# Kernel optimization log

Hardware: AMD Instinct MI355X
Metric: run time of the kernel (lower is better)

The kernel has to match this reference:

```python
import jax, jax.numpy as jnp
import numpy as np

VERY_NEG = -1e30

H = 768           # hidden_size
A_DIM = 768       # attention_dim_size
N_TREE = 40000    # num_tree_nodes (embed_init vocab)
N_CODES = 10000   # number of leaf codes (rows of leaves_list)
MAX_ANC = 8       # max ancestors per code
B, V, M = 16, 32, 48  # batch, visits, codes per visit
OUT = 512         # classifier output_size


def setup_inputs() -> dict:
    key = jax.random.key(0)
    ks = jax.random.split(key, 12)
    leaves_list = jax.random.randint(ks[0], (N_CODES, MAX_ANC), 0, N_TREE)
    ancestors_list = jax.random.randint(ks[1], (N_CODES, MAX_ANC), 0, N_TREE)
    masks = (jax.random.uniform(ks[2], (N_CODES, MAX_ANC)) > 0.3).astype(jnp.float32)
    masks = masks.at[:, 0].set(1.0)  # ensure at least one valid ancestor
    input_ids = jax.random.randint(ks[3], (B, V, M), 0, N_CODES + 1)  # 0 is padding row
    code_mask = (jax.random.uniform(ks[4], (B, V, M)) > 0.2).astype(jnp.float32)
    code_mask = code_mask.at[:, :, 0].set(1.0)
    s = 1.0 / np.sqrt(H)
    embed_table = jax.random.normal(ks[5], (N_TREE, H), dtype=jnp.float32) * s
    w1 = jax.random.normal(ks[6], (2 * H, A_DIM), dtype=jnp.float32) * (1.0 / np.sqrt(2 * H))
    b1 = jnp.zeros((A_DIM,), dtype=jnp.float32)
    w2 = jax.random.normal(ks[7], (A_DIM, 1), dtype=jnp.float32) * (1.0 / np.sqrt(A_DIM))
    b2 = jnp.zeros((1,), dtype=jnp.float32)
    wc = jax.random.normal(ks[8], (H, OUT), dtype=jnp.float32) * s
    bc = jnp.zeros((OUT,), dtype=jnp.float32)
    return {
        "embed_table": embed_table, "w1": w1, "b1": b1, "w2": w2, "b2": b2,
        "wc": wc, "bc": bc, "masks": masks, "code_mask": code_mask,
        "leaves_list": leaves_list, "ancestors_list": ancestors_list,
        "input_ids": input_ids,
    }


def reference(embed_table, w1, b1, w2, b2, wc, bc, masks, code_mask,
              leaves_list, ancestors_list, input_ids):
    # --- DAGAttention2D over ancestor axis ---
    leaves = embed_table[leaves_list]        # [N, A, H]
    ancestors = embed_table[ancestors_list]  # [N, A, H]
    m = masks[:, :, None]                    # [N, A, 1]
    x = jnp.concatenate([leaves * m, ancestors * m], axis=-1)  # [N, A, 2H]
    x = jax.nn.relu(jnp.einsum('nah,hd->nad', x, w1) + b1)
    x = jnp.einsum('nad,do->nao', x, w2) + b2                  # [N, A, 1]
    x = x + (1.0 - m) * VERY_NEG
    attn = jax.nn.softmax(x, axis=1)                           # softmax over ancestors
    dag_emb = (attn * ancestors * m).sum(axis=1)               # [N, H]
    # --- dict_matrix with padding row 0, embedding lookup ---
    dict_matrix = jnp.concatenate([jnp.zeros((1, dag_emb.shape[1]), dag_emb.dtype), dag_emb], axis=0)
    emb = dict_matrix[input_ids]             # [B, V, M, H]
    cm = code_mask[..., None]
    pooled = (emb * cm).sum(axis=2) / jnp.clip(cm.sum(axis=2), 1.0, None)  # [B, V, H]
    # --- Classifier (dropout inactive at eval, activation=None) ---
    out = jnp.einsum('bvh,ho->bvo', pooled, wc) + bc           # [B, V, OUT]
    return out
```

## Files before the change

### kernel.cpp

```cpp
#include <hip/hip_runtime.h>
#include <stdint.h>

typedef unsigned short u16;
typedef __bf16 bfx8 __attribute__((ext_vector_type(8)));
typedef float f32x4 __attribute__((ext_vector_type(4)));

#define HD 768
#define NTREE 40000
#define NCODES 10000
#define GNN 1536
#define OUTD 512
#define NBV 512
#define VNEG (-1e30f)
#define TB 4

#define BM 256
#define BN 256
#define BK 64
#define NKT (HD / BK)
#define NMT ((NTREE + BM - 1) / BM)
#define NNT (GNN / BN)
#define GRID (NMT * NNT)
#define Q8 (GRID / 8)
#define R8 (GRID % 8)

#define WAITV(n) asm volatile("s_waitcnt vmcnt(" #n ")" ::: "memory")
#define LGKM(n)  asm volatile("s_waitcnt lgkmcnt(" #n ")" ::: "memory")

__device__ __forceinline__ float bf2f(u16 u) {
  union { uint32_t i; float f; } v; v.i = ((uint32_t)u) << 16; return v.f;
}
__device__ __forceinline__ u16 f2bf(float f) {
  union { float fl; uint32_t i; } v; v.fl = f;
  uint32_t u = v.i;
  u += 0x7FFFu + ((u >> 16) & 1u);
  return (u16)(u >> 16);
}

#define NBLK_CONV 30000
__global__ void k_prep(const float* __restrict__ E, u16* __restrict__ Ebf,
                       const float* __restrict__ w1, u16* __restrict__ Bt) {
  const int bid = blockIdx.x, tid = threadIdx.x;
  if (bid < NBLK_CONV) {
    const int i = bid * 256 + tid;
    float4 v = ((const float4*)E)[i];
    ushort4 r;
    r.x = f2bf(v.x); r.y = f2bf(v.y); r.z = f2bf(v.z); r.w = f2bf(v.w);
    ((ushort4*)Ebf)[i] = r;
  } else {
    const int idx = (bid - NBLK_CONV) * 256 + tid;
    if (idx < GNN * HD) {
      const int n = idx / HD, k = idx % HD;
      const int srow = k + ((n >= HD) ? HD : 0);
      const int scol = (n >= HD) ? (n - HD) : n;
      Bt[idx] = f2bf(w1[(size_t)srow * HD + scol]);
    }
  }
}

__global__ __launch_bounds__(512, 2) void k_gemm(const u16* __restrict__ A,
                                                 const u16* __restrict__ B,
                                                 u16* __restrict__ C) {
  __shared__ u16 lds[65536];

  const int tid    = threadIdx.x;
  const int lane   = tid & 63;
  const int wv     = tid >> 6;
  const int wr     = wv >> 2;
  const int wc     = wv & 3;
  const int lane15 = lane & 15;
  const int g      = lane >> 4;

  const int orig = blockIdx.x;
  const int xcd = orig & 7, lin = orig >> 3;
  const int wg = (xcd < R8 ? xcd * (Q8 + 1) : R8 * (Q8 + 1) + (xcd - R8) * Q8) + lin;
  const int mt = wg / NNT, nt = wg % NNT;
  const int tm = mt * BM, tn = nt * BN;

  uint32_t aOff[2][2], bOff[2][2];
#pragma unroll
  for (int u = 0; u < 2; ++u) {
    const int o    = u * 8192 + tid * 16;
    const int rloc = o >> 7;
    const int c    = ((o >> 4) & 7) ^ (rloc & 7);
#pragma unroll
    for (int h = 0; h < 2; ++h) {
      int ra = tm + h * 128 + rloc; if (ra > NTREE - 1) ra = NTREE - 1;
      aOff[u][h] = (uint32_t)ra * HD + c * 8;
      bOff[u][h] = (uint32_t)(tn + h * 128 + rloc) * HD + c * 8;
    }
  }

#define STAGE_A(MH, NB, TT) do {                                               \
    _Pragma("unroll") for (int u = 0; u < 2; ++u)                              \
      __builtin_amdgcn_global_load_lds(                                        \
        (const __attribute__((address_space(1))) void*)(A + aOff[u][MH] + (TT) * BK), \
        (__attribute__((address_space(3))) void*)((char*)lds + (NB) * 32768 +  \
            (MH) * 16384 + u * 8192 + tid * 16),                               \
        16, 0, 0);                                                             \
  } while (0)

#define STAGE_B(NH, NB, TT) do {                                               \
    _Pragma("unroll") for (int u = 0; u < 2; ++u)                              \
      __builtin_amdgcn_global_load_lds(                                        \
        (const __attribute__((address_space(1))) void*)(B + bOff[u][NH] + (TT) * BK), \
        (__attribute__((address_space(3))) void*)((char*)lds + 65536 +         \
            (NB) * 32768 + (NH) * 16384 + u * 8192 + tid * 16),                \
        16, 0, 0);                                                             \
  } while (0)

  f32x4 acc[4][4][2];
#pragma unroll
  for (int q = 0; q < 4; ++q)
#pragma unroll
    for (int i = 0; i < 4; ++i)
#pragma unroll
      for (int j = 0; j < 2; ++j) acc[q][i][j] = (f32x4){0.f, 0.f, 0.f, 0.f};

  int colz[2];
  colz[0] = ((0 * 4 + g) ^ (lane15 & 7)) * 8;
  colz[1] = ((1 * 4 + g) ^ (lane15 & 7)) * 8;
  const int aLane = wr * 4096 + lane15 * 64;
  const int bLane = wc * 2048 + lane15 * 64;

  bfx8 aF[4][2], bF[2][2];

#define READ_A(MH, BA) do {                                                    \
    _Pragma("unroll") for (int mf = 0; mf < 4; ++mf)                           \
      _Pragma("unroll") for (int ks = 0; ks < 2; ++ks)                         \
        aF[mf][ks] = *(const bfx8*)&lds[(BA) + (MH) * 8192 + aLane +           \
                                        mf * 1024 + colz[ks]];                 \
  } while (0)

#define READ_B(NH, BB) do {                                                    \
    _Pragma("unroll") for (int nf = 0; nf < 2; ++nf)                           \
      _Pragma("unroll") for (int ks = 0; ks < 2; ++ks)                         \
        bF[nf][ks] = *(const bfx8*)&lds[(BB) + (NH) * 8192 + bLane +           \
                                        nf * 1024 + colz[ks]];                 \
  } while (0)

#define MFMA_Q(Q) do {                                                         \
    LGKM(0);                                                                   \
    __builtin_amdgcn_sched_barrier(0);                                         \
    __builtin_amdgcn_s_setprio(1);                                             \
    _Pragma("unroll") for (int mf = 0; mf < 4; ++mf)                           \
      _Pragma("unroll") for (int nf = 0; nf < 2; ++nf)                         \
        _Pragma("unroll") for (int ks = 0; ks < 2; ++ks)                       \
          acc[Q][mf][nf] = __builtin_amdgcn_mfma_f32_16x16x32_bf16(            \
              aF[mf][ks], bF[nf][ks], acc[Q][mf][nf], 0, 0, 0);                \
    __builtin_amdgcn_s_setprio(0);                                             \
  } while (0)

  STAGE_A(0, 0, 0);
  STAGE_B(0, 0, 0);
  STAGE_B(1, 0, 0);
  STAGE_A(1, 0, 0);
  WAITV(4);
  __builtin_amdgcn_s_barrier();

  for (int t = 0; t < NKT; ++t) {
    const int bA = (t & 1) * 16384;
    const int bB = 32768 + (t & 1) * 16384;
    const int nb = (t + 1) & 1;
    const bool more = (t + 1 < NKT);

    READ_A(0, bA);
    READ_B(0, bB);
    if (more) STAGE_A(0, nb, t + 1);
    MFMA_Q(0);
    if (more) { WAITV(4); } else { WAITV(2); }
    __builtin_amdgcn_s_barrier();

    READ_B(1, bB);
    if (more) STAGE_B(0, nb, t + 1);
    MFMA_Q(1);
    if (more) { WAITV(4); } else { WAITV(0); }
    __builtin_amdgcn_s_barrier();

    READ_A(1, bA);
    if (more) STAGE_B(1, nb, t + 1);
    MFMA_Q(2);
    __builtin_amdgcn_s_barrier();

    READ_B(0, bB);
    if (more) STAGE_A(1, nb, t + 1);
    MFMA_Q(3);
    if (more) { WAITV(4); }
    __builtin_amdgcn_s_barrier();
  }

  const int r0 = (lane >> 4) * 4, cc = lane15;
  const int qmh[4] = {0, 0, 1, 1}, qnh[4] = {0, 1, 1, 0};
#pragma unroll
  for (int q = 0; q < 4; ++q) {
#pragma unroll
    for (int mf = 0; mf < 4; ++mf) {
#pragma unroll
      for (int nf = 0; nf < 2; ++nf) {
#pragma unroll
        for (int rr = 0; rr < 4; ++rr) {
          const int row = tm + qmh[q] * 128 + wr * 64 + mf * 16 + r0 + rr;
          if (row < NTREE) {
            const int col = tn + qnh[q] * 128 + wc * 32 + nf * 16 + cc;
            C[(size_t)row * GNN + col] = f2bf(acc[q][mf][nf][rr]);
          }
        }
      }
    }
  }
#undef MFMA_Q
#undef READ_A
#undef READ_B
#undef STAGE_A
#undef STAGE_B
}

__global__ __launch_bounds__(512) void k_attn(const u16* __restrict__ PQ,
                                              const u16* __restrict__ Ebf,
                                              const float* __restrict__ b1,
                                              const float* __restrict__ w2,
                                              const float* __restrict__ b2,
                                              const float* __restrict__ masks,
                                              const int* __restrict__ leaves,
                                              const int* __restrict__ anc,
                                              u16* __restrict__ dag) {
  const int n = blockIdx.x;
  const int tid = threadIdx.x, lane = tid & 63, wv = tid >> 6;
  __shared__ float sc[8];
  __shared__ float m_s[8];
  __shared__ int   an_s[8];
  __shared__ int   lv_s[8];
  if (tid < 8) {
    an_s[tid] = anc[n * 8 + tid];
    lv_s[tid] = leaves[n * 8 + tid];
    m_s[tid]  = masks[n * 8 + tid];
  }
  __syncthreads();

  {
    const int a = wv;
    const float mm = m_s[a];
    if (mm == 0.f) {
      if (lane == 0) sc[a] = VNEG;
    } else {
      const int l = lv_s[a], an = an_s[a];
      const u16* pr = PQ + (size_t)l * GNN;
      const u16* qr = PQ + (size_t)an * GNN + HD;
      const int d0 = lane * 12;
      float s = 0.f;
#pragma unroll
      for (int jj = 0; jj < 3; ++jj) {
        const int d = d0 + jj * 4;
        ushort4 pv = *(const ushort4*)(pr + d);
        ushort4 qv = *(const ushort4*)(qr + d);
        float4  bb = *(const float4*)(b1 + d);
        float4  ww = *(const float4*)(w2 + d);
        float v;
        v = fmaxf(bf2f(pv.x) + bf2f(qv.x) + bb.x, 0.f); s += v * ww.x;
        v = fmaxf(bf2f(pv.y) + bf2f(qv.y) + bb.y, 0.f); s += v * ww.y;
        v = fmaxf(bf2f(pv.z) + bf2f(qv.z) + bb.z, 0.f); s += v * ww.z;
        v = fmaxf(bf2f(pv.w) + bf2f(qv.w) + bb.w, 0.f); s += v * ww.w;
      }
#pragma unroll
      for (int off = 32; off > 0; off >>= 1) s += __shfl_down(s, off);
      if (lane == 0) sc[a] = s + b2[0];
    }
  }
  __syncthreads();

  float mx = sc[0];
#pragma unroll
  for (int a = 1; a < 8; ++a) mx = fmaxf(mx, sc[a]);
  float ex[8], den = 0.f;
#pragma unroll
  for (int a = 0; a < 8; ++a) { ex[a] = expf(sc[a] - mx); den += ex[a]; }
  const float inv = 1.0f / den;
  float cf[8];
#pragma unroll
  for (int a = 0; a < 8; ++a) cf[a] = ex[a] * inv * m_s[a];

  if (tid < 384) {
    const int d = tid * 2;
    float a0 = 0.f, a1 = 0.f;
#pragma unroll
    for (int a = 0; a < 8; ++a) {
      const float cfa = cf[a];
      if (cfa != 0.f) {
        const uint32_t w = *(const uint32_t*)(Ebf + (size_t)an_s[a] * HD + d);
        a0 += cfa * bf2f((u16)(w & 0xffffu));
        a1 += cfa * bf2f((u16)(w >> 16));
      }
    }
    const uint32_t packed = (uint32_t)f2bf(a0) | ((uint32_t)f2bf(a1) << 16);
    *(uint32_t*)(dag + (size_t)n * HD + d) = packed;
  }
}

__global__ __launch_bounds__(256) void k_pool(const u16* __restrict__ dag,
                                              const int* __restrict__ ids,
                                              const float* __restrict__ cm,
                                              float* __restrict__ pooled) {
  const int bv = blockIdx.x, tid = threadIdx.x;
  __shared__ int   id_s[48];
  __shared__ float cm_s[48];
  if (tid < 48) { id_s[tid] = ids[bv * 48 + tid]; cm_s[tid] = cm[bv * 48 + tid]; }
  __syncthreads();
  float cnt = 0.f;
  for (int m = 0; m < 48; ++m) cnt += cm_s[m];
  const float scale = 1.0f / fmaxf(cnt, 1.0f);
  if (tid < 192) {
    float4 accv = make_float4(0.f, 0.f, 0.f, 0.f);
    for (int m = 0; m < 48; ++m) {
      const int id = id_s[m];
      const float cv = cm_s[m];
      if (id > 0 && cv != 0.f) {
        ushort4 v = *(const ushort4*)(dag + (size_t)(id - 1) * HD + tid * 4);
        accv.x += cv * bf2f(v.x); accv.y += cv * bf2f(v.y);
        accv.z += cv * bf2f(v.z); accv.w += cv * bf2f(v.w);
      }
    }
    accv.x *= scale; accv.y *= scale; accv.z *= scale; accv.w *= scale;
    *(float4*)(pooled + (size_t)bv * HD + tid * 4) = accv;
  }
}

__global__ __launch_bounds__(256) void k_out(const float* __restrict__ pooled,
                                             const float* __restrict__ wc,
                                             const float* __restrict__ bc,
                                             float* __restrict__ out) {
  const int b0 = blockIdx.x * TB;
  const int tid = threadIdx.x;
  __shared__ float pl[TB][HD];
  for (int i = tid; i < TB * HD; i += 256) pl[i / HD][i % HD] = pooled[(size_t)b0 * HD + i];
  __syncthreads();
  float a0[TB], a1[TB];
#pragma unroll
  for (int r = 0; r < TB; ++r) { a0[r] = 0.f; a1[r] = 0.f; }
  for (int h = 0; h < HD; ++h) {
    const float w0  = wc[(size_t)h * OUTD + tid];
    const float w1v = wc[(size_t)h * OUTD + tid + 256];
#pragma unroll
    for (int r = 0; r < TB; ++r) { const float p = pl[r][h]; a0[r] += p * w0; a1[r] += p * w1v; }
  }
  const float bc0 = bc[tid], bc1 = bc[tid + 256];
#pragma unroll
  for (int r = 0; r < TB; ++r) {
    out[(size_t)(b0 + r) * OUTD + tid]       = a0[r] + bc0;
    out[(size_t)(b0 + r) * OUTD + tid + 256] = a1[r] + bc1;
  }
}

extern "C" void kernel_launch(void* const* d_in, const int* in_sizes, int n_in,
                              void* d_out, int out_size, void* d_ws, size_t ws_size,
                              hipStream_t stream) {
  const float* E     = (const float*)d_in[0];
  const float* w1    = (const float*)d_in[1];
  const float* b1    = (const float*)d_in[2];
  const float* w2    = (const float*)d_in[3];
  const float* b2    = (const float*)d_in[4];
  const float* wc    = (const float*)d_in[5];
  const float* bc    = (const float*)d_in[6];
  const float* masks = (const float*)d_in[7];
  const float* cm    = (const float*)d_in[8];
  const int*   leaves = (const int*)d_in[9];
  const int*   anc    = (const int*)d_in[10];
  const int*   ids    = (const int*)d_in[11];
  float* out = (float*)d_out;

  if (n_in < 12) return;
  if (in_sizes[0] != NTREE * HD) return;
  if (out_size != NBV * OUTD) return;

  char* ws = (char*)d_ws;
  const size_t szEbf = (size_t)NTREE * HD * 2;
  const size_t szBt  = (size_t)GNN * HD * 2;
  const size_t szPQ  = (size_t)NTREE * GNN * 2;
  const size_t szDag = (size_t)NCODES * HD * 2;
  const size_t szPl  = (size_t)NBV * HD * 4;
  if (ws_size < szEbf + szBt + szPQ + szDag + szPl) return;

  u16*   Ebf    = (u16*)ws;            ws += szEbf;
  u16*   Bt     = (u16*)ws;            ws += szBt;
  u16*   PQ     = (u16*)ws;            ws += szPQ;
  u16*   dag    = (u16*)ws;            ws += szDag;
  float* pooled = (float*)ws;          ws += szPl;

  const int nPrep = NBLK_CONV + (GNN * HD + 255) / 256;
  k_prep<<<nPrep, 256, 0, stream>>>(E, Ebf, w1, Bt);
  k_gemm<<<GRID, 512, 0, stream>>>(Ebf, Bt, PQ);
  k_attn<<<NCODES, 512, 0, stream>>>(PQ, Ebf, b1, w2, b2, masks, leaves, anc, dag);
  k_pool<<<NBV, 256, 0, stream>>>(dag, ids, cm, pooled);
  k_out<<<NBV / TB, 256, 0, stream>>>(pooled, wc, bc, out);
}
```

Before: 277.0 us.

## Retile projection GEMM, vectorize attention score loads, and tile classifier GEMM

The main bf16 GEMM moves from 256x256x64 tiles with 512 threads and double buffering to 128x256x32 tiles with 256 threads and a three-stage LDS ring buffer, changing the swizzle and the wait/barrier schedule. The attention kernel now loads PQ rows as 8-wide and 4-wide vectors per lane instead of three 4-wide loads, so it issues fewer memory instructions. The classifier kernel becomes a shared-memory tiled 64x64 GEMM over 64 blocks in place of the row-strip loop. Together these aim to improve GEMM occupancy and latency hiding and to raise parallelism in the small final GEMM, at the cost of lower per-block reuse in the main GEMM.

```diff
diff --git a/kernel.cpp b/kernel.cpp
--- a/kernel.cpp
+++ b/kernel.cpp
@@ -4,6 +4,7 @@
 typedef unsigned short u16;
 typedef __bf16 bfx8 __attribute__((ext_vector_type(8)));
 typedef float f32x4 __attribute__((ext_vector_type(4)));
+typedef u16 u16x8 __attribute__((ext_vector_type(8)));
 
 #define HD 768
 #define NTREE 40000
@@ -12,20 +13,18 @@
 #define OUTD 512
 #define NBV 512
 #define VNEG (-1e30f)
-#define TB 4
-
-#define BM 256
-#define BN 256
-#define BK 64
-#define NKT (HD / BK)
-#define NMT ((NTREE + BM - 1) / BM)
-#define NNT (GNN / BN)
-#define GRID (NMT * NNT)
-#define Q8 (GRID / 8)
-#define R8 (GRID % 8)
+
+#define BM2 128
+#define BN2 256
+#define BK2 32
+#define NKT2 (HD / BK2)
+#define NMT2 ((NTREE + BM2 - 1) / BM2)
+#define NNT2 (GNN / BN2)
+#define GRID2 (NMT2 * NNT2)
+#define Q82 (GRID2 / 8)
+#define R82 (GRID2 % 8)
 
 #define WAITV(n) asm volatile("s_waitcnt vmcnt(" #n ")" ::: "memory")
-#define LGKM(n)  asm volatile("s_waitcnt lgkmcnt(" #n ")" ::: "memory")
 
 __device__ __forceinline__ float bf2f(u16 u) {
   union { uint32_t i; float f; } v; v.i = ((uint32_t)u) << 16; return v.f;
@@ -58,161 +57,145 @@
   }
 }
 
-__global__ __launch_bounds__(512, 2) void k_gemm(const u16* __restrict__ A,
+__global__ __launch_bounds__(256, 2) void k_gemm(const u16* __restrict__ A,
                                                  const u16* __restrict__ B,
                                                  u16* __restrict__ C) {
-  __shared__ u16 lds[65536];
+  __shared__ u16 lds[36864];
 
   const int tid    = threadIdx.x;
   const int lane   = tid & 63;
   const int wv     = tid >> 6;
-  const int wr     = wv >> 2;
-  const int wc     = wv & 3;
+  const int wr     = wv >> 1;
+  const int wc     = wv & 1;
   const int lane15 = lane & 15;
   const int g      = lane >> 4;
 
   const int orig = blockIdx.x;
   const int xcd = orig & 7, lin = orig >> 3;
-  const int wg = (xcd < R8 ? xcd * (Q8 + 1) : R8 * (Q8 + 1) + (xcd - R8) * Q8) + lin;
-  const int mt = wg / NNT, nt = wg % NNT;
-  const int tm = mt * BM, tn = nt * BN;
-
-  uint32_t aOff[2][2], bOff[2][2];
+  const int wg = (xcd < R82 ? xcd * (Q82 + 1)
+                            : R82 * (Q82 + 1) + (xcd - R82) * Q82) + lin;
+  const int mt = wg / NNT2, nt = wg % NNT2;
+  const int tm = mt * BM2, tn = nt * BN2;
+
+  uint32_t aOff[2], bOff[4];
 #pragma unroll
   for (int u = 0; u < 2; ++u) {
-    const int o    = u * 8192 + tid * 16;
-    const int rloc = o >> 7;
-    const int c    = ((o >> 4) & 7) ^ (rloc & 7);
-#pragma unroll
-    for (int h = 0; h < 2; ++h) {
-      int ra = tm + h * 128 + rloc; if (ra > NTREE - 1) ra = NTREE - 1;
-      aOff[u][h] = (uint32_t)ra * HD + c * 8;
-      bOff[u][h] = (uint32_t)(tn + h * 128 + rloc) * HD + c * 8;
-    }
-  }
-
-#define STAGE_A(MH, NB, TT) do {                                               \
+    const int idx = u * 256 + tid;
+    const int r = idx >> 2, ph = idx & 3, c = ph ^ (r & 3);
+    int ra = tm + r; if (ra > NTREE - 1) ra = NTREE - 1;
+    aOff[u] = (uint32_t)ra * HD + c * 8;
+  }
+#pragma unroll
+  for (int u = 0; u < 4; ++u) {
+    const int idx = u * 256 + tid;
+    const int r = idx >> 2, ph = idx & 3, c = ph ^ (r & 3);
+    bOff[u] = (uint32_t)(tn + r) * HD + c * 8;
+  }
+
+#define GLL(SRC, DSTBYTE)                                                      \
+  __builtin_amdgcn_global_load_lds(                                            \
+      (const __attribute__((address_space(1))) void*)(SRC),                    \
+      (__attribute__((address_space(3))) void*)((char*)lds + (DSTBYTE)),       \
+      16, 0, 0)
+
+#define STAGE_A(TT, BI) do {                                                   \
     _Pragma("unroll") for (int u = 0; u < 2; ++u)                              \
-      __builtin_amdgcn_global_load_lds(                                        \
-        (const __attribute__((address_space(1))) void*)(A + aOff[u][MH] + (TT) * BK), \
-        (__attribute__((address_space(3))) void*)((char*)lds + (NB) * 32768 +  \
-            (MH) * 16384 + u * 8192 + tid * 16),                               \
-        16, 0, 0);                                                             \
+      GLL(A + aOff[u] + (TT) * BK2, (BI) * 24576 + (u * 256 + tid) * 16);      \
   } while (0)
-
-#define STAGE_B(NH, NB, TT) do {                                               \
-    _Pragma("unroll") for (int u = 0; u < 2; ++u)                              \
-      __builtin_amdgcn_global_load_lds(                                        \
-        (const __attribute__((address_space(1))) void*)(B + bOff[u][NH] + (TT) * BK), \
-        (__attribute__((address_space(3))) void*)((char*)lds + 65536 +         \
-            (NB) * 32768 + (NH) * 16384 + u * 8192 + tid * 16),                \
-        16, 0, 0);                                                             \
+#define STAGE_BE(TT, BI) do {                                                  \
+    _Pragma("unroll") for (int u = 0; u < 4; u += 2)                           \
+      GLL(B + bOff[u] + (TT) * BK2,                                            \
+          (BI) * 24576 + 8192 + (u * 256 + tid) * 16);                         \
   } while (0)
-
-  f32x4 acc[4][4][2];
-#pragma unroll
-  for (int q = 0; q < 4; ++q)
-#pragma unroll
-    for (int i = 0; i < 4; ++i)
-#pragma unroll
-      for (int j = 0; j < 2; ++j) acc[q][i][j] = (f32x4){0.f, 0.f, 0.f, 0.f};
-
-  int colz[2];
-  colz[0] = ((0 * 4 + g) ^ (lane15 & 7)) * 8;
-  colz[1] = ((1 * 4 + g) ^ (lane15 & 7)) * 8;
-  const int aLane = wr * 4096 + lane15 * 64;
-  const int bLane = wc * 2048 + lane15 * 64;
-
-  bfx8 aF[4][2], bF[2][2];
-
-#define READ_A(MH, BA) do {                                                    \
-    _Pragma("unroll") for (int mf = 0; mf < 4; ++mf)                           \
-      _Pragma("unroll") for (int ks = 0; ks < 2; ++ks)                         \
-        aF[mf][ks] = *(const bfx8*)&lds[(BA) + (MH) * 8192 + aLane +           \
-                                        mf * 1024 + colz[ks]];                 \
+#define STAGE_BO(TT, BI) do {                                                  \
+    _Pragma("unroll") for (int u = 1; u < 4; u += 2)                           \
+      GLL(B + bOff[u] + (TT) * BK2,                                            \
+          (BI) * 24576 + 8192 + (u * 256 + tid) * 16);                         \
   } while (0)
 
-#define READ_B(NH, BB) do {                                                    \
-    _Pragma("unroll") for (int nf = 0; nf < 2; ++nf)                           \
-      _Pragma("unroll") for (int ks = 0; ks < 2; ++ks)                         \
-        bF[nf][ks] = *(const bfx8*)&lds[(BB) + (NH) * 8192 + bLane +           \
-                                        nf * 1024 + colz[ks]];                 \
-  } while (0)
-
-#define MFMA_Q(Q) do {                                                         \
-    LGKM(0);                                                                   \
-    __builtin_amdgcn_sched_barrier(0);                                         \
-    __builtin_amdgcn_s_setprio(1);                                             \
-    _Pragma("unroll") for (int mf = 0; mf < 4; ++mf)                           \
-      _Pragma("unroll") for (int nf = 0; nf < 2; ++nf)                         \
-        _Pragma("unroll") for (int ks = 0; ks < 2; ++ks)                       \
-          acc[Q][mf][nf] = __builtin_amdgcn_mfma_f32_16x16x32_bf16(            \
-              aF[mf][ks], bF[nf][ks], acc[Q][mf][nf], 0, 0, 0);                \
-    __builtin_amdgcn_s_setprio(0);                                             \
-  } while (0)
-
-  STAGE_A(0, 0, 0);
-  STAGE_B(0, 0, 0);
-  STAGE_B(1, 0, 0);
-  STAGE_A(1, 0, 0);
-  WAITV(4);
+  f32x4 acc[4][8];
+#pragma unroll
+  for (int i = 0; i < 4; ++i)
+#pragma unroll
+    for (int j = 0; j < 8; ++j) acc[i][j] = (f32x4){0.f, 0.f, 0.f, 0.f};
+
+  int aIdx[4], bIdx[8];
+#pragma unroll
+  for (int mf = 0; mf < 4; ++mf) {
+    const int R = wr * 64 + mf * 16 + lane15;
+    aIdx[mf] = R * 32 + ((g ^ (R & 3)) << 3);
+  }
+#pragma unroll
+  for (int nf = 0; nf < 8; ++nf) {
+    const int R = wc * 128 + nf * 16 + lane15;
+    bIdx[nf] = 4096 + R * 32 + ((g ^ (R & 3)) << 3);
+  }
+
+  STAGE_A(0, 0); STAGE_BE(0, 0); STAGE_BO(0, 0);
+  STAGE_A(1, 1); STAGE_BE(1, 1); STAGE_BO(1, 1);
+  WAITV(8);
   __builtin_amdgcn_s_barrier();
 
-  for (int t = 0; t < NKT; ++t) {
-    const int bA = (t & 1) * 16384;
-    const int bB = 32768 + (t & 1) * 16384;
-    const int nb = (t + 1) & 1;
-    const bool more = (t + 1 < NKT);
-
-    READ_A(0, bA);
-    READ_B(0, bB);
-    if (more) STAGE_A(0, nb, t + 1);
-    MFMA_Q(0);
-    if (more) { WAITV(4); } else { WAITV(2); }
+  int rb = 0, sb = 2;
+  for (int t = 0; t < NKT2; ++t) {
+    const int bu = rb * 12288;
+    const bool more = (t + 2 < NKT2);
+    bfx8 aF[4], bF[4], bG[4];
+
+#pragma unroll
+    for (int mf = 0; mf < 4; ++mf) aF[mf] = *(const bfx8*)&lds[bu + aIdx[mf]];
+#pragma unroll
+    for (int nf = 0; nf < 4; ++nf) bF[nf] = *(const bfx8*)&lds[bu + bIdx[nf]];
+    if (more) STAGE_A(t + 2, sb);
+    __builtin_amdgcn_s_setprio(1);
+#pragma unroll
+    for (int mf = 0; mf < 4; ++mf)
+#pragma unroll
+      for (int nf = 0; nf < 4; ++nf)
+        acc[mf][nf] = __builtin_amdgcn_mfma_f32_16x16x32_bf16(
+            aF[mf], bF[nf], acc[mf][nf], 0, 0, 0);
+    __builtin_amdgcn_s_setprio(0);
+    if (t < NKT2 - 2) { WAITV(8); } else { WAITV(0); }
     __builtin_amdgcn_s_barrier();
 
-    READ_B(1, bB);
-    if (more) STAGE_B(0, nb, t + 1);
-    MFMA_Q(1);
-    if (more) { WAITV(4); } else { WAITV(0); }
+#pragma unroll
+    for (int nf = 0; nf < 4; ++nf) bG[nf] = *(const bfx8*)&lds[bu + bIdx[4 + nf]];
+    if (more) { STAGE_BE(t + 2, sb); STAGE_BO(t + 2, sb); }
+    __builtin_amdgcn_s_setprio(1);
+#pragma unroll
+    for (int mf = 0; mf < 4; ++mf)
+#pragma unroll
+      for (int nf = 0; nf < 4; ++nf)
+        acc[mf][4 + nf] = __builtin_amdgcn_mfma_f32_16x16x32_bf16(
+            aF[mf], bG[nf], acc[mf][4 + nf], 0, 0, 0);
+    __builtin_amdgcn_s_setprio(0);
+    if (t < NKT2 - 2) { WAITV(8); }
+    else if (t == NKT2 - 2) { WAITV(0); }
     __builtin_amdgcn_s_barrier();
 
-    READ_A(1, bA);
-    if (more) STAGE_B(1, nb, t + 1);
-    MFMA_Q(2);
-    __builtin_amdgcn_s_barrier();
-
-    READ_B(0, bB);
-    if (more) STAGE_A(1, nb, t + 1);
-    MFMA_Q(3);
-    if (more) { WAITV(4); }
-    __builtin_amdgcn_s_barrier();
-  }
-
-  const int r0 = (lane >> 4) * 4, cc = lane15;
-  const int qmh[4] = {0, 0, 1, 1}, qnh[4] = {0, 1, 1, 0};
-#pragma unroll
-  for (int q = 0; q < 4; ++q) {
-#pragma unroll
-    for (int mf = 0; mf < 4; ++mf) {
-#pragma unroll
-      for (int nf = 0; nf < 2; ++nf) {
-#pragma unroll
-        for (int rr = 0; rr < 4; ++rr) {
-          const int row = tm + qmh[q] * 128 + wr * 64 + mf * 16 + r0 + rr;
-          if (row < NTREE) {
-            const int col = tn + qnh[q] * 128 + wc * 32 + nf * 16 + cc;
-            C[(size_t)row * GNN + col] = f2bf(acc[q][mf][nf][rr]);
-          }
+    rb = (rb == 2) ? 0 : rb + 1;
+    sb = (sb == 2) ? 0 : sb + 1;
+  }
+
+  const int r0 = (lane >> 4) * 4;
+#pragma unroll
+  for (int mf = 0; mf < 4; ++mf) {
+#pragma unroll
+    for (int nf = 0; nf < 8; ++nf) {
+#pragma unroll
+      for (int rr = 0; rr < 4; ++rr) {
+        const int row = tm + wr * 64 + mf * 16 + r0 + rr;
+        if (row < NTREE) {
+          const int col = tn + wc * 128 + nf * 16 + lane15;
+          C[(size_t)row * GNN + col] = f2bf(acc[mf][nf][rr]);
         }
       }
     }
   }
-#undef MFMA_Q
-#undef READ_A
-#undef READ_B
 #undef STAGE_A
-#undef STAGE_B
+#undef STAGE_BE
+#undef STAGE_BO
+#undef GLL
 }
 
 __global__ __launch_bounds__(512) void k_attn(const u16* __restrict__ PQ,
@@ -246,21 +229,29 @@
       const int l = lv_s[a], an = an_s[a];
       const u16* pr = PQ + (size_t)l * GNN;
       const u16* qr = PQ + (size_t)an * GNN + HD;
-      const int d0 = lane * 12;
-      float s = 0.f;
-#pragma unroll
-      for (int jj = 0; jj < 3; ++jj) {
-        const int d = d0 + jj * 4;
-        ushort4 pv = *(const ushort4*)(pr + d);
-        ushort4 qv = *(const ushort4*)(qr + d);
-        float4  bb = *(const float4*)(b1 + d);
-        float4  ww = *(const float4*)(w2 + d);
-        float v;
-        v = fmaxf(bf2f(pv.x) + bf2f(qv.x) + bb.x, 0.f); s += v * ww.x;
-        v = fmaxf(bf2f(pv.y) + bf2f(qv.y) + bb.y, 0.f); s += v * ww.y;
-        v = fmaxf(bf2f(pv.z) + bf2f(qv.z) + bb.z, 0.f); s += v * ww.z;
-        v = fmaxf(bf2f(pv.w) + bf2f(qv.w) + bb.w, 0.f); s += v * ww.w;
-      }
+      u16x8  p1 = *(const u16x8*)(pr + lane * 8);
+      u16x8  q1 = *(const u16x8*)(qr + lane * 8);
+      ushort4 p2 = *(const ushort4*)(pr + 512 + lane * 4);
+      ushort4 q2 = *(const ushort4*)(qr + 512 + lane * 4);
+      const float4 bbA = *(const float4*)(b1 + lane * 8);
+      const float4 bbB = *(const float4*)(b1 + lane * 8 + 4);
+      const float4 bbC = *(const float4*)(b1 + 512 + lane * 4);
+      const float4 wwA = *(const float4*)(w2 + lane * 8);
+      const float4 wwB = *(const float4*)(w2 + lane * 8 + 4);
+      const float4 wwC = *(const float4*)(w2 + 512 + lane * 4);
+      float s = 0.f, v;
+      v = fmaxf(bf2f(p1[0]) + bf2f(q1[0]) + bbA.x, 0.f); s += v * wwA.x;
+      v = fmaxf(bf2f(p1[1]) + bf2f(q1[1]) + bbA.y, 0.f); s += v * wwA.y;
+      v = fmaxf(bf2f(p1[2]) + bf2f(q1[2]) + bbA.z, 0.f); s += v * wwA.z;
+      v = fmaxf(bf2f(p1[3]) + bf2f(q1[3]) + bbA.w, 0.f); s += v * wwA.w;
+      v = fmaxf(bf2f(p1[4]) + bf2f(q1[4]) + bbB.x, 0.f); s += v * wwB.x;
+      v = fmaxf(bf2f(p1[5]) + bf2f(q1[5]) + bbB.y, 0.f); s += v * wwB.y;
+      v = fmaxf(bf2f(p1[6]) + bf2f(q1[6]) + bbB.z, 0.f); s += v * wwB.z;
+      v = fmaxf(bf2f(p1[7]) + bf2f(q1[7]) + bbB.w, 0.f); s += v * wwB.w;
+      v = fmaxf(bf2f(p2.x) + bf2f(q2.x) + bbC.x, 0.f);   s += v * wwC.x;
+      v = fmaxf(bf2f(p2.y) + bf2f(q2.y) + bbC.y, 0.f);   s += v * wwC.y;
+      v = fmaxf(bf2f(p2.z) + bf2f(q2.z) + bbC.z, 0.f);   s += v * wwC.z;
+      v = fmaxf(bf2f(p2.w) + bf2f(q2.w) + bbC.w, 0.f);   s += v * wwC.w;
 #pragma unroll
       for (int off = 32; off > 0; off >>= 1) s += __shfl_down(s, off);
       if (lane == 0) sc[a] = s + b2[0];
@@ -328,25 +319,53 @@
                                              const float* __restrict__ wc,
                                              const float* __restrict__ bc,
                                              float* __restrict__ out) {
-  const int b0 = blockIdx.x * TB;
+  const int rb = blockIdx.x >> 3, cb = blockIdx.x & 7;
   const int tid = threadIdx.x;
-  __shared__ float pl[TB][HD];
-  for (int i = tid; i < TB * HD; i += 256) pl[i / HD][i % HD] = pooled[(size_t)b0 * HD + i];
-  __syncthreads();
-  float a0[TB], a1[TB];
-#pragma unroll
-  for (int r = 0; r < TB; ++r) { a0[r] = 0.f; a1[r] = 0.f; }
-  for (int h = 0; h < HD; ++h) {
-    const float w0  = wc[(size_t)h * OUTD + tid];
-    const float w1v = wc[(size_t)h * OUTD + tid + 256];
-#pragma unroll
-    for (int r = 0; r < TB; ++r) { const float p = pl[r][h]; a0[r] += p * w0; a1[r] += p * w1v; }
-  }
-  const float bc0 = bc[tid], bc1 = bc[tid + 256];
-#pragma unroll
-  for (int r = 0; r < TB; ++r) {
-    out[(size_t)(b0 + r) * OUTD + tid]       = a0[r] + bc0;
-    out[(size_t)(b0 + r) * OUTD + tid + 256] = a1[r] + bc1;
+  const int ty = tid >> 4, tx = tid & 15;
+  __shared__ float pl[64][33];
+  __shared__ float wcs[32][64];
+  float acc[4][4];
+#pragma unroll
+  for (int i = 0; i < 4; ++i)
+#pragma unroll
+    for (int j = 0; j < 4; ++j) acc[i][j] = 0.f;
+
+  for (int kt = 0; kt < HD / 32; ++kt) {
+    __syncthreads();
+#pragma unroll
+    for (int u = 0; u < 2; ++u) {
+      const int i = u * 256 + tid;
+      const int r = i >> 3, kq = (i & 7) * 4;
+      float4 v = *(const float4*)(pooled + (size_t)(rb * 64 + r) * HD + kt * 32 + kq);
+      pl[r][kq] = v.x; pl[r][kq + 1] = v.y; pl[r][kq + 2] = v.z; pl[r][kq + 3] = v.w;
+    }
+#pragma unroll
+    for (int u = 0; u < 2; ++u) {
+      const int i = u * 256 + tid;
+      const int k = i >> 4, cq = (i & 15) * 4;
+      *(float4*)&wcs[k][cq] =
+          *(const float4*)(wc + (size_t)(kt * 32 + k) * OUTD + cb * 64 + cq);
+    }
+    __syncthreads();
+#pragma unroll 8
+    for (int k = 0; k < 32; ++k) {
+      const float a0 = pl[ty * 4 + 0][k], a1 = pl[ty * 4 + 1][k];
+      const float a2 = pl[ty * 4 + 2][k], a3 = pl[ty * 4 + 3][k];
+      const float4 b = *(const float4*)&wcs[k][tx * 4];
+      acc[0][0] += a0 * b.x; acc[0][1] += a0 * b.y; acc[0][2] += a0 * b.z; acc[0][3] += a0 * b.w;
+      acc[1][0] += a1 * b.x; acc[1][1] += a1 * b.y; acc[1][2] += a1 * b.z; acc[1][3] += a1 * b.w;
+      acc[2][0] += a2 * b.x; acc[2][1] += a2 * b.y; acc[2][2] += a2 * b.z; acc[2][3] += a2 * b.w;
+      acc[3][0] += a3 * b.x; acc[3][1] += a3 * b.y; acc[3][2] += a3 * b.z; acc[3][3] += a3 * b.w;
+    }
+  }
+#pragma unroll
+  for (int i = 0; i < 4; ++i) {
+#pragma unroll
+    for (int j = 0; j < 4; ++j) {
+      const int row = rb * 64 + ty * 4 + i;
+      const int col = cb * 64 + tx * 4 + j;
+      out[(size_t)row * OUTD + col] = acc[i][j] + bc[col];
+    }
   }
 }
 
@@ -387,8 +406,8 @@
 
   const int nPrep = NBLK_CONV + (GNN * HD + 255) / 256;
   k_prep<<<nPrep, 256, 0, stream>>>(E, Ebf, w1, Bt);
-  k_gemm<<<GRID, 512, 0, stream>>>(Ebf, Bt, PQ);
+  k_gemm<<<GRID2, 256, 0, stream>>>(Ebf, Bt, PQ);
   k_attn<<<NCODES, 512, 0, stream>>>(PQ, Ebf, b1, w2, b2, masks, leaves, anc, dag);
   k_pool<<<NBV, 256, 0, stream>>>(dag, ids, cm, pooled);
-  k_out<<<NBV / TB, 256, 0, stream>>>(pooled, wc, bc, out);
-}
+  k_out<<<64, 256, 0, stream>>>(pooled, wc, bc, out);
+}
```

Result: slower. 283.4 us (+2.3%).
